# Kernel tuning notes

Measured on AMD Instinct MI355X. Metric: run time of the kernel, lower is better.

Reference implementation:

```python
import jax, jax.numpy as jnp
import numpy as np

B, S, DIM = 2, 1024, 1024
E, K, INTER = 16, 2, 512
SHARED_INTER = 2 * INTER  # n_shared_experts * moe_inter_dim
ROUTE_SCALE = 1.0


def setup_inputs() -> dict:
    key = jax.random.key(0)
    ks = jax.random.split(key, 8)
    init = lambda k, shape: jax.random.normal(k, shape, dtype=jnp.float32) * 0.02
    return {
        "x": jax.random.normal(ks[0], (B, S, DIM), dtype=jnp.float32),
        "gate_w": init(ks[1], (E, DIM)),
        "w1": init(ks[2], (E, INTER, DIM)),
        "w2": init(ks[3], (E, DIM, INTER)),
        "w3": init(ks[4], (E, INTER, DIM)),
        "sw1": init(ks[5], (SHARED_INTER, DIM)),
        "sw2": init(ks[6], (DIM, SHARED_INTER)),
        "sw3": init(ks[7], (SHARED_INTER, DIM)),
    }


def reference(x, gate_w, w1, w2, w3, sw1, sw2, sw3):
    b, s, d = x.shape
    xt = x.reshape(-1, d)            # [T, D] flattened tokens
    T = xt.shape[0]

    # Gate: sigmoid scores, top-k experts, normalize selected weights
    scores = jax.nn.sigmoid(xt @ gate_w.T)           # [T, E]
    topv, topi = jax.lax.top_k(scores, K)            # [T, K]
    weights = topv / jnp.sum(topv, axis=-1, keepdims=True) * ROUTE_SCALE

    # Per-token dense combine weights over experts: gate[t, e]
    gate = jnp.zeros((T, E), xt.dtype).at[jnp.arange(T)[:, None], topi].add(weights)

    # Routed experts (SwiGLU), computed densely and combined with gate weights
    h = jax.nn.silu(jnp.einsum('td,eid->tei', xt, w1)) * jnp.einsum('td,eid->tei', xt, w3)
    expert_out = jnp.einsum('tei,edi->ted', h, w2)   # [T, E, D]
    y = jnp.einsum('ted,te->td', expert_out, gate)   # [T, D]

    # Shared expert (SwiGLU MLP over all tokens)
    z = (jax.nn.silu(xt @ sw1.T) * (xt @ sw3.T)) @ sw2.T

    return (y + z).reshape(b, s, d)
```

## Files before the change

### kernel.cpp

```cpp
#include <hip/hip_runtime.h>
#include <stdint.h>

typedef unsigned short u16;
typedef __bf16 bf16x8 __attribute__((ext_vector_type(8)));
typedef float f32x4 __attribute__((ext_vector_type(4)));

#define TTOK 2048
#define DIMSZ 1024
#define NROUT 16
#define INTERSZ 512

__device__ __forceinline__ u16 f2bf(float f) {
    unsigned int u = __builtin_bit_cast(unsigned int, f);
    unsigned int r = u + 0x7FFFu + ((u >> 16) & 1u);
    return (u16)(r >> 16);
}

__device__ __forceinline__ void gl2lds16(const void* g, void* l) {
    __builtin_amdgcn_global_load_lds(
        (const __attribute__((address_space(1))) void*)(uintptr_t)g,
        (__attribute__((address_space(3))) void*)(uintptr_t)l,
        16, 0, 0);
}

#define NA4 (NROUT * INTERSZ * DIMSZ / 4)
#define NB4 (DIMSZ * DIMSZ / 4)
#define NR4 (NA4 + NB4)
__global__ void cast_all(const float* __restrict__ w1, const float* __restrict__ sw1,
                         const float* __restrict__ w3, const float* __restrict__ sw3,
                         const float* __restrict__ w2, const float* __restrict__ sw2,
                         u16* __restrict__ W1b, u16* __restrict__ W3b,
                         u16* __restrict__ W2b) {
    const int n4 = 3 * NR4;
    for (int i = blockIdx.x * blockDim.x + threadIdx.x; i < n4;
         i += gridDim.x * blockDim.x) {
        int r = i / NR4;
        int j = i - r * NR4;
        const float* a; const float* b; u16* d;
        if (r == 0)      { a = w1; b = sw1; d = W1b; }
        else if (r == 1) { a = w3; b = sw3; d = W3b; }
        else             { a = w2; b = sw2; d = W2b; }
        float4 v = (j < NA4) ? ((const float4*)a)[j] : ((const float4*)b)[j - NA4];
        ushort4 o;
        o.x = f2bf(v.x); o.y = f2bf(v.y); o.z = f2bf(v.z); o.w = f2bf(v.w);
        *(ushort4*)&d[(size_t)j * 4] = o;
    }
}

__global__ __launch_bounds__(256) void gate_score(
    const float* __restrict__ x, const float* __restrict__ gw,
    int* __restrict__ topi, float2* __restrict__ topw, u16* __restrict__ Xbf) {
    const int t = blockIdx.x;
    const int tid = threadIdx.x;
    const int wave = tid >> 6, lane = tid & 63;
    const int d0 = tid * 4;
    float4 xv = *(const float4*)(x + (size_t)t * DIMSZ + d0);
    ushort4 o;
    o.x = f2bf(xv.x); o.y = f2bf(xv.y); o.z = f2bf(xv.z); o.w = f2bf(xv.w);
    *(ushort4*)&Xbf[(size_t)t * DIMSZ + d0] = o;

    float acc[16];
    #pragma unroll
    for (int e = 0; e < 16; ++e) {
        float4 g = *(const float4*)(gw + e * DIMSZ + d0);
        acc[e] = xv.x * g.x + xv.y * g.y + xv.z * g.z + xv.w * g.w;
    }
    #pragma unroll
    for (int off = 32; off > 0; off >>= 1) {
        #pragma unroll
        for (int e = 0; e < 16; ++e) acc[e] += __shfl_xor(acc[e], off);
    }
    __shared__ float part[4][16];
    __shared__ float sfin[16];
    if (lane < 16) part[wave][lane] = acc[lane];
    __syncthreads();
    if (wave == 0 && lane < 16) {
        float s = part[0][lane] + part[1][lane] + part[2][lane] + part[3][lane];
        sfin[lane] = 1.f / (1.f + expf(-s));
    }
    __syncthreads();
    if (tid == 0) {
        int i0 = 0; float v0 = sfin[0];
        #pragma unroll
        for (int e = 1; e < 16; ++e) { float v = sfin[e]; if (v > v0) { v0 = v; i0 = e; } }
        int i1 = -1; float v1 = -1e30f;
        #pragma unroll
        for (int e = 0; e < 16; ++e) { float v = sfin[e]; if (e != i0 && v > v1) { v1 = v; i1 = e; } }
        float inv = 1.f / (v0 + v1);
        topi[t] = i0 | (i1 << 8);
        topw[t] = make_float2(v0 * inv, v1 * inv);
    }
}

__global__ __launch_bounds__(256) void route_kernel(
    const int* __restrict__ topi, const float2* __restrict__ topw,
    int* __restrict__ counts, int* __restrict__ tokidx, float* __restrict__ tokw) {
    const int e = blockIdx.x;
    const int tid = threadIdx.x;
    int p[8]; int m[8]; int cnt = 0;
    #pragma unroll
    for (int j = 0; j < 8; ++j) {
        int t = tid * 8 + j;
        p[j] = topi[t];
        m[j] = ((p[j] & 255) == e) || ((p[j] >> 8) == e) ? 1 : 0;
        cnt += m[j];
    }
    const int lane = tid & 63, wave = tid >> 6;
    int v = cnt;
    #pragma unroll
    for (int off = 1; off < 64; off <<= 1) {
        int u = __shfl_up(v, off);
        if (lane >= off) v += u;
    }
    __shared__ int wsum[4];
    if (lane == 63) wsum[wave] = v;
    __syncthreads();
    int wbase = 0;
    #pragma unroll
    for (int w = 0; w < 4; ++w) wbase += (w < wave) ? wsum[w] : 0;
    int base = wbase + v - cnt;
    #pragma unroll
    for (int j = 0; j < 8; ++j) {
        if (m[j]) {
            int t = tid * 8 + j;
            float2 w2 = topw[t];
            tokidx[e * TTOK + base] = t;
            tokw[e * TTOK + base] = ((p[j] & 255) == e) ? w2.x : w2.y;
            ++base;
        }
    }
    if (tid == 0) counts[e] = wsum[0] + wsum[1] + wsum[2] + wsum[3];
}

__global__ __launch_bounds__(256) void gemm1s(
    const u16* __restrict__ Xbf, const u16* __restrict__ W1b,
    const u16* __restrict__ W3b, const int* __restrict__ counts,
    const int* __restrict__ tokidx, const float* __restrict__ tokw,
    u16* __restrict__ Hc, u16* __restrict__ Hs) {
    const int e = blockIdx.z;
    const int cnt = (e < NROUT) ? counts[e] : TTOK;
    const int m0 = blockIdx.y * 64;
    if (m0 >= cnt) return;
    const int n0 = blockIdx.x * 64;
    __shared__ u16 As[64 * 64], B1s[64 * 64], B3s[64 * 64];
    const size_t eoff = (size_t)e * INTERSZ * DIMSZ;
    const u16* B1 = W1b + eoff + (size_t)n0 * DIMSZ;
    const u16* B3 = W3b + eoff + (size_t)n0 * DIMSZ;
    const int tid = threadIdx.x;

    int rowi[2], cgsi[2]; size_t arow[2];
    #pragma unroll
    for (int i = 0; i < 2; ++i) {
        int c = tid + i * 256;
        rowi[i] = c >> 3;
        cgsi[i] = ((c & 7) ^ (rowi[i] & 7)) * 8;
        int slot = m0 + rowi[i];
        int g;
        if (e < NROUT) g = (slot < cnt) ? tokidx[e * TTOK + slot] : 0;
        else           g = slot;
        arow[i] = (size_t)g * DIMSZ;
    }
    f32x4 acc1[2][2] = {}; f32x4 acc3[2][2] = {};
    const int wave = tid >> 6, lane = tid & 63;
    const int wm = (wave >> 1) * 32, wn = (wave & 1) * 32;
    const int lr = lane & 15, lq = lane >> 4;

    for (int kt = 0; kt < DIMSZ / 64; ++kt) {
        const int k0 = kt * 64;
        #pragma unroll
        for (int i = 0; i < 2; ++i) {
            int c = tid + i * 256;
            int boff = rowi[i] * DIMSZ + k0 + cgsi[i];
            gl2lds16(Xbf + arow[i] + k0 + cgsi[i], &As[c * 8]);
            gl2lds16(B1 + boff, &B1s[c * 8]);
            gl2lds16(B3 + boff, &B3s[c * 8]);
        }
        __syncthreads();
        #pragma unroll
        for (int ks = 0; ks < 2; ++ks) {
            bf16x8 af[2], b1f[2], b3f[2];
            const int g = lq + ks * 4;
            #pragma unroll
            for (int mt = 0; mt < 2; ++mt) {
                int m = wm + mt * 16 + lr;
                af[mt] = *(const bf16x8*)&As[(m * 8 + (g ^ (m & 7))) * 8];
            }
            #pragma unroll
            for (int nt = 0; nt < 2; ++nt) {
                int n = wn + nt * 16 + lr;
                int ch = (n * 8 + (g ^ (n & 7))) * 8;
                b1f[nt] = *(const bf16x8*)&B1s[ch];
                b3f[nt] = *(const bf16x8*)&B3s[ch];
            }
            #pragma unroll
            for (int mt = 0; mt < 2; ++mt) {
                #pragma unroll
                for (int nt = 0; nt < 2; ++nt) {
                    acc1[mt][nt] = __builtin_amdgcn_mfma_f32_16x16x32_bf16(af[mt], b1f[nt], acc1[mt][nt], 0, 0, 0);
                    acc3[mt][nt] = __builtin_amdgcn_mfma_f32_16x16x32_bf16(af[mt], b3f[nt], acc3[mt][nt], 0, 0, 0);
                }
            }
        }
        __syncthreads();
    }
    #pragma unroll
    for (int mt = 0; mt < 2; ++mt) {
        #pragma unroll
        for (int nt = 0; nt < 2; ++nt) {
            #pragma unroll
            for (int r = 0; r < 4; ++r) {
                int m = wm + mt * 16 + lq * 4 + r;
                int n = wn + nt * 16 + lr;
                int slot = m0 + m;
                bool valid = slot < cnt;
                float h1 = acc1[mt][nt][r], h3 = acc3[mt][nt][r];
                float hv = 0.f;
                if (valid) {
                    float tw = (e < NROUT) ? tokw[e * TTOK + slot] : 1.0f;
                    hv = h1 / (1.f + __expf(-h1)) * h3 * tw;
                }
                if (e < NROUT)
                    Hc[((size_t)e * TTOK + slot) * INTERSZ + n0 + n] = f2bf(hv);
                else
                    Hs[(size_t)slot * DIMSZ + (e - NROUT) * INTERSZ + n0 + n] = f2bf(hv);
            }
        }
    }
}

__global__ __launch_bounds__(256) void gemm2_shared(
    const u16* __restrict__ Hs, const u16* __restrict__ W2sb,
    float* __restrict__ out) {
    __shared__ u16 As[64 * 64], Bs[64 * 64];
    const int m0 = blockIdx.y * 64, n0 = blockIdx.x * 64;
    const u16* A0 = Hs + (size_t)m0 * DIMSZ;
    const u16* B0 = W2sb + (size_t)n0 * DIMSZ;
    const int tid = threadIdx.x;
    const int wave = tid >> 6, lane = tid & 63;
    const int wm = (wave >> 1) * 32, wn = (wave & 1) * 32;
    const int lr = lane & 15, lq = lane >> 4;

    f32x4 acc[2][2] = {};
    for (int kt = 0; kt < DIMSZ / 64; ++kt) {
        const int k0 = kt * 64;
        #pragma unroll
        for (int i = 0; i < 2; ++i) {
            int c = tid + i * 256;
            int row = c >> 3;
            int cgs = ((c & 7) ^ (row & 7)) * 8;
            gl2lds16(A0 + (size_t)row * DIMSZ + k0 + cgs, &As[c * 8]);
            gl2lds16(B0 + (size_t)row * DIMSZ + k0 + cgs, &Bs[c * 8]);
        }
        __syncthreads();
        #pragma unroll
        for (int ks = 0; ks < 2; ++ks) {
            bf16x8 af[2], bfr[2];
            const int g = lq + ks * 4;
            #pragma unroll
            for (int mt = 0; mt < 2; ++mt) {
                int m = wm + mt * 16 + lr;
                af[mt] = *(const bf16x8*)&As[(m * 8 + (g ^ (m & 7))) * 8];
            }
            #pragma unroll
            for (int nt = 0; nt < 2; ++nt) {
                int n = wn + nt * 16 + lr;
                bfr[nt] = *(const bf16x8*)&Bs[(n * 8 + (g ^ (n & 7))) * 8];
            }
            #pragma unroll
            for (int mt = 0; mt < 2; ++mt) {
                #pragma unroll
                for (int nt = 0; nt < 2; ++nt) {
                    acc[mt][nt] = __builtin_amdgcn_mfma_f32_16x16x32_bf16(af[mt], bfr[nt], acc[mt][nt], 0, 0, 0);
                }
            }
        }
        __syncthreads();
    }
    #pragma unroll
    for (int mt = 0; mt < 2; ++mt) {
        #pragma unroll
        for (int nt = 0; nt < 2; ++nt) {
            #pragma unroll
            for (int r = 0; r < 4; ++r) {
                int m = wm + mt * 16 + lq * 4 + r;
                int n = wn + nt * 16 + lr;
                out[(size_t)(m0 + m) * DIMSZ + n0 + n] = acc[mt][nt][r];
            }
        }
    }
}

__global__ __launch_bounds__(256) void gemm2_routed(
    const u16* __restrict__ Hc, const u16* __restrict__ W2b,
    const int* __restrict__ counts, const int* __restrict__ tokidx,
    float* __restrict__ out) {
    const int e = blockIdx.z;
    const int cnt = counts[e];
    const int m0 = blockIdx.y * 64;
    if (m0 >= cnt) return;
    const int n0 = blockIdx.x * 64;
    __shared__ u16 As[64 * 64], Bs[64 * 64];
    const u16* A0 = Hc + ((size_t)e * TTOK + m0) * INTERSZ;
    const u16* B0 = W2b + ((size_t)e * DIMSZ + n0) * INTERSZ;
    const int tid = threadIdx.x;
    const int wave = tid >> 6, lane = tid & 63;
    const int wm = (wave >> 1) * 32, wn = (wave & 1) * 32;
    const int lr = lane & 15, lq = lane >> 4;

    f32x4 acc[2][2] = {};
    for (int kt = 0; kt < INTERSZ / 64; ++kt) {
        const int k0 = kt * 64;
        #pragma unroll
        for (int i = 0; i < 2; ++i) {
            int c = tid + i * 256;
            int row = c >> 3;
            int cgs = ((c & 7) ^ (row & 7)) * 8;
            gl2lds16(A0 + (size_t)row * INTERSZ + k0 + cgs, &As[c * 8]);
            gl2lds16(B0 + (size_t)row * INTERSZ + k0 + cgs, &Bs[c * 8]);
        }
        __syncthreads();
        #pragma unroll
        for (int ks = 0; ks < 2; ++ks) {
            bf16x8 af[2], bfr[2];
            const int g = lq + ks * 4;
            #pragma unroll
            for (int mt = 0; mt < 2; ++mt) {
                int m = wm + mt * 16 + lr;
                af[mt] = *(const bf16x8*)&As[(m * 8 + (g ^ (m & 7))) * 8];
            }
            #pragma unroll
            for (int nt = 0; nt < 2; ++nt) {
                int n = wn + nt * 16 + lr;
                bfr[nt] = *(const bf16x8*)&Bs[(n * 8 + (g ^ (n & 7))) * 8];
            }
            #pragma unroll
            for (int mt = 0; mt < 2; ++mt) {
                #pragma unroll
                for (int nt = 0; nt < 2; ++nt) {
                    acc[mt][nt] = __builtin_amdgcn_mfma_f32_16x16x32_bf16(af[mt], bfr[nt], acc[mt][nt], 0, 0, 0);
                }
            }
        }
        __syncthreads();
    }
    #pragma unroll
    for (int mt = 0; mt < 2; ++mt) {
        #pragma unroll
        for (int r = 0; r < 4; ++r) {
            int m = wm + mt * 16 + lq * 4 + r;
            int slot = m0 + m;
            if (slot < cnt) {
                int t = tokidx[e * TTOK + slot];
                #pragma unroll
                for (int nt = 0; nt < 2; ++nt) {
                    int n = wn + nt * 16 + lr;
                    unsafeAtomicAdd(&out[(size_t)t * DIMSZ + n0 + n], acc[mt][nt][r]);
                }
            }
        }
    }
}

extern "C" void kernel_launch(void* const* d_in, const int* in_sizes, int n_in,
                              void* d_out, int out_size, void* d_ws, size_t ws_size,
                              hipStream_t stream) {
    const float* x      = (const float*)d_in[0];
    const float* gate_w = (const float*)d_in[1];
    const float* w1     = (const float*)d_in[2];
    const float* w2     = (const float*)d_in[3];
    const float* w3     = (const float*)d_in[4];
    const float* sw1    = (const float*)d_in[5];
    const float* sw2    = (const float*)d_in[6];
    const float* sw3    = (const float*)d_in[7];
    float* out = (float*)d_out;

    char* ws = (char*)d_ws;
    const size_t SZ_W   = (size_t)(NROUT + 2) * INTERSZ * DIMSZ * 2;
    const size_t SZ_XBF = (size_t)TTOK * DIMSZ * 2;
    u16*   W1b    = (u16*)(ws);
    u16*   W3b    = (u16*)(ws + SZ_W);
    u16*   W2all  = (u16*)(ws + 2 * SZ_W);
    u16*   Xbf    = (u16*)(ws + 3 * SZ_W);
    char*  route  = ws + 3 * SZ_W + SZ_XBF;
    int*   counts = (int*)route;
    int*   topi   = (int*)(route + 256);
    float2* topw  = (float2*)(route + 256 + TTOK * 4);
    int*   tokidx = (int*)(route + 256 + TTOK * 12);
    float* tokw   = (float*)(route + 256 + TTOK * 12 + 16 * TTOK * 4);
    char*  hbuf   = route + 256 + TTOK * 12 + 2 * (size_t)16 * TTOK * 4;
    u16*   Hc     = (u16*)hbuf;
    u16*   Hs     = (u16*)(hbuf + (size_t)NROUT * TTOK * INTERSZ * 2);
    u16*   W2sb   = W2all + (size_t)NROUT * DIMSZ * INTERSZ;

    cast_all<<<8192, 256, 0, stream>>>(w1, sw1, w3, sw3, w2, sw2, W1b, W3b, W2all);
    gate_score<<<TTOK, 256, 0, stream>>>(x, gate_w, topi, topw, Xbf);
    route_kernel<<<NROUT, 256, 0, stream>>>(topi, topw, counts, tokidx, tokw);
    gemm1s<<<dim3(INTERSZ / 64, TTOK / 64, NROUT + 2), 256, 0, stream>>>(
        Xbf, W1b, W3b, counts, tokidx, tokw, Hc, Hs);
    gemm2_shared<<<dim3(DIMSZ / 64, TTOK / 64), 256, 0, stream>>>(Hs, W2sb, out);
    gemm2_routed<<<dim3(DIMSZ / 64, TTOK / 64, NROUT), 256, 0, stream>>>(
        Hc, W2all, counts, tokidx, out);
}
```

Measured before the change: 238.5 us.

## Widen gemm1 N-tile, merge shared and routed gemm2 kernels, vectorize weight cast

gemm1s now computes a 64x128 tile per block, reusing each gathered activation tile across twice as many output columns and halving the number of redundant A loads. The shared and routed second GEMMs are merged into one launch that accumulates with atomics into an output zeroed by a memset, so they can run concurrently instead of back-to-back. The weight cast kernel uses a 2D grid with one row per weight group and 8-element vector stores, which removes the per-element division. The changes add register and LDS pressure in gemm1, atomic traffic for the shared expert, and one extra memset.

```diff
diff --git a/kernel.cpp b/kernel.cpp
--- a/kernel.cpp
+++ b/kernel.cpp
@@ -4,6 +4,7 @@
 typedef unsigned short u16;
 typedef __bf16 bf16x8 __attribute__((ext_vector_type(8)));
 typedef float f32x4 __attribute__((ext_vector_type(4)));
+typedef unsigned short u16x8 __attribute__((ext_vector_type(8)));
 
 #define TTOK 2048
 #define DIMSZ 1024
@@ -25,25 +26,27 @@
 
 #define NA4 (NROUT * INTERSZ * DIMSZ / 4)
 #define NB4 (DIMSZ * DIMSZ / 4)
-#define NR4 (NA4 + NB4)
+#define NA8 (NA4 / 2)
+#define NR8 ((NA4 + NB4) / 2)
 __global__ void cast_all(const float* __restrict__ w1, const float* __restrict__ sw1,
                          const float* __restrict__ w3, const float* __restrict__ sw3,
                          const float* __restrict__ w2, const float* __restrict__ sw2,
                          u16* __restrict__ W1b, u16* __restrict__ W3b,
                          u16* __restrict__ W2b) {
-    const int n4 = 3 * NR4;
-    for (int i = blockIdx.x * blockDim.x + threadIdx.x; i < n4;
-         i += gridDim.x * blockDim.x) {
-        int r = i / NR4;
-        int j = i - r * NR4;
-        const float* a; const float* b; u16* d;
-        if (r == 0)      { a = w1; b = sw1; d = W1b; }
-        else if (r == 1) { a = w3; b = sw3; d = W3b; }
-        else             { a = w2; b = sw2; d = W2b; }
-        float4 v = (j < NA4) ? ((const float4*)a)[j] : ((const float4*)b)[j - NA4];
-        ushort4 o;
-        o.x = f2bf(v.x); o.y = f2bf(v.y); o.z = f2bf(v.z); o.w = f2bf(v.w);
-        *(ushort4*)&d[(size_t)j * 4] = o;
+    const int r = blockIdx.y;
+    const float* a; const float* b; u16* d;
+    if (r == 0)      { a = w1; b = sw1; d = W1b; }
+    else if (r == 1) { a = w3; b = sw3; d = W3b; }
+    else             { a = w2; b = sw2; d = W2b; }
+    for (int j = blockIdx.x * blockDim.x + threadIdx.x; j < NR8;
+         j += gridDim.x * blockDim.x) {
+        const float4* src = (j < NA8) ? (const float4*)a + 2 * (size_t)j
+                                      : (const float4*)b + 2 * (size_t)(j - NA8);
+        float4 v0 = src[0], v1 = src[1];
+        u16x8 o;
+        o[0] = f2bf(v0.x); o[1] = f2bf(v0.y); o[2] = f2bf(v0.z); o[3] = f2bf(v0.w);
+        o[4] = f2bf(v1.x); o[5] = f2bf(v1.y); o[6] = f2bf(v1.z); o[7] = f2bf(v1.w);
+        *(u16x8*)&d[(size_t)j * 8] = o;
     }
 }
 
@@ -141,28 +144,35 @@
     const int cnt = (e < NROUT) ? counts[e] : TTOK;
     const int m0 = blockIdx.y * 64;
     if (m0 >= cnt) return;
-    const int n0 = blockIdx.x * 64;
-    __shared__ u16 As[64 * 64], B1s[64 * 64], B3s[64 * 64];
+    const int n0 = blockIdx.x * 128;
+    __shared__ u16 As[64 * 64], B1s[128 * 64], B3s[128 * 64];
     const size_t eoff = (size_t)e * INTERSZ * DIMSZ;
     const u16* B1 = W1b + eoff + (size_t)n0 * DIMSZ;
     const u16* B3 = W3b + eoff + (size_t)n0 * DIMSZ;
     const int tid = threadIdx.x;
 
-    int rowi[2], cgsi[2]; size_t arow[2];
+    int rowa[2], cgsa[2]; size_t arow[2];
     #pragma unroll
     for (int i = 0; i < 2; ++i) {
         int c = tid + i * 256;
-        rowi[i] = c >> 3;
-        cgsi[i] = ((c & 7) ^ (rowi[i] & 7)) * 8;
-        int slot = m0 + rowi[i];
+        rowa[i] = c >> 3;
+        cgsa[i] = ((c & 7) ^ (rowa[i] & 7)) * 8;
+        int slot = m0 + rowa[i];
         int g;
         if (e < NROUT) g = (slot < cnt) ? tokidx[e * TTOK + slot] : 0;
         else           g = slot;
         arow[i] = (size_t)g * DIMSZ;
     }
-    f32x4 acc1[2][2] = {}; f32x4 acc3[2][2] = {};
+    int rowb[4], cgsb[4];
+    #pragma unroll
+    for (int i = 0; i < 4; ++i) {
+        int c = tid + i * 256;
+        rowb[i] = c >> 3;
+        cgsb[i] = ((c & 7) ^ (rowb[i] & 7)) * 8;
+    }
+    f32x4 acc1[2][4] = {}; f32x4 acc3[2][4] = {};
     const int wave = tid >> 6, lane = tid & 63;
-    const int wm = (wave >> 1) * 32, wn = (wave & 1) * 32;
+    const int wm = (wave >> 1) * 32, wn = (wave & 1) * 64;
     const int lr = lane & 15, lq = lane >> 4;
 
     for (int kt = 0; kt < DIMSZ / 64; ++kt) {
@@ -170,15 +180,19 @@
         #pragma unroll
         for (int i = 0; i < 2; ++i) {
             int c = tid + i * 256;
-            int boff = rowi[i] * DIMSZ + k0 + cgsi[i];
-            gl2lds16(Xbf + arow[i] + k0 + cgsi[i], &As[c * 8]);
+            gl2lds16(Xbf + arow[i] + k0 + cgsa[i], &As[c * 8]);
+        }
+        #pragma unroll
+        for (int i = 0; i < 4; ++i) {
+            int c = tid + i * 256;
+            int boff = rowb[i] * DIMSZ + k0 + cgsb[i];
             gl2lds16(B1 + boff, &B1s[c * 8]);
             gl2lds16(B3 + boff, &B3s[c * 8]);
         }
         __syncthreads();
         #pragma unroll
         for (int ks = 0; ks < 2; ++ks) {
-            bf16x8 af[2], b1f[2], b3f[2];
+            bf16x8 af[2], b1f[4], b3f[4];
             const int g = lq + ks * 4;
             #pragma unroll
             for (int mt = 0; mt < 2; ++mt) {
@@ -186,7 +200,7 @@
                 af[mt] = *(const bf16x8*)&As[(m * 8 + (g ^ (m & 7))) * 8];
             }
             #pragma unroll
-            for (int nt = 0; nt < 2; ++nt) {
+            for (int nt = 0; nt < 4; ++nt) {
                 int n = wn + nt * 16 + lr;
                 int ch = (n * 8 + (g ^ (n & 7))) * 8;
                 b1f[nt] = *(const bf16x8*)&B1s[ch];
@@ -195,7 +209,7 @@
             #pragma unroll
             for (int mt = 0; mt < 2; ++mt) {
                 #pragma unroll
-                for (int nt = 0; nt < 2; ++nt) {
+                for (int nt = 0; nt < 4; ++nt) {
                     acc1[mt][nt] = __builtin_amdgcn_mfma_f32_16x16x32_bf16(af[mt], b1f[nt], acc1[mt][nt], 0, 0, 0);
                     acc3[mt][nt] = __builtin_amdgcn_mfma_f32_16x16x32_bf16(af[mt], b3f[nt], acc3[mt][nt], 0, 0, 0);
                 }
@@ -206,7 +220,7 @@
     #pragma unroll
     for (int mt = 0; mt < 2; ++mt) {
         #pragma unroll
-        for (int nt = 0; nt < 2; ++nt) {
+        for (int nt = 0; nt < 4; ++nt) {
             #pragma unroll
             for (int r = 0; r < 4; ++r) {
                 int m = wm + mt * 16 + lq * 4 + r;
@@ -228,28 +242,44 @@
     }
 }
 
-__global__ __launch_bounds__(256) void gemm2_shared(
-    const u16* __restrict__ Hs, const u16* __restrict__ W2sb,
+__global__ __launch_bounds__(256) void gemm2u(
+    const u16* __restrict__ Hc, const u16* __restrict__ Hs,
+    const u16* __restrict__ W2b, const u16* __restrict__ W2sb,
+    const int* __restrict__ counts, const int* __restrict__ tokidx,
     float* __restrict__ out) {
+    const int e = blockIdx.z;
+    const bool routed = (e < NROUT);
+    const int cnt = routed ? counts[e] : TTOK;
+    const int m0 = blockIdx.y * 64;
+    if (m0 >= cnt) return;
+    const int n0 = blockIdx.x * 64;
+    const int klen = routed ? INTERSZ : DIMSZ;
     __shared__ u16 As[64 * 64], Bs[64 * 64];
-    const int m0 = blockIdx.y * 64, n0 = blockIdx.x * 64;
-    const u16* A0 = Hs + (size_t)m0 * DIMSZ;
-    const u16* B0 = W2sb + (size_t)n0 * DIMSZ;
+    const u16* A0 = routed ? Hc + ((size_t)e * TTOK + m0) * INTERSZ
+                           : Hs + (size_t)m0 * DIMSZ;
+    const u16* B0 = routed ? W2b + ((size_t)e * DIMSZ + n0) * INTERSZ
+                           : W2sb + (size_t)n0 * DIMSZ;
     const int tid = threadIdx.x;
     const int wave = tid >> 6, lane = tid & 63;
     const int wm = (wave >> 1) * 32, wn = (wave & 1) * 32;
     const int lr = lane & 15, lq = lane >> 4;
 
+    int rowi[2], cgsi[2];
+    #pragma unroll
+    for (int i = 0; i < 2; ++i) {
+        int c = tid + i * 256;
+        rowi[i] = c >> 3;
+        cgsi[i] = ((c & 7) ^ (rowi[i] & 7)) * 8;
+    }
+
     f32x4 acc[2][2] = {};
-    for (int kt = 0; kt < DIMSZ / 64; ++kt) {
+    for (int kt = 0; kt < klen / 64; ++kt) {
         const int k0 = kt * 64;
         #pragma unroll
         for (int i = 0; i < 2; ++i) {
             int c = tid + i * 256;
-            int row = c >> 3;
-            int cgs = ((c & 7) ^ (row & 7)) * 8;
-            gl2lds16(A0 + (size_t)row * DIMSZ + k0 + cgs, &As[c * 8]);
-            gl2lds16(B0 + (size_t)row * DIMSZ + k0 + cgs, &Bs[c * 8]);
+            gl2lds16(A0 + (size_t)rowi[i] * klen + k0 + cgsi[i], &As[c * 8]);
+            gl2lds16(B0 + (size_t)rowi[i] * klen + k0 + cgsi[i], &Bs[c * 8]);
         }
         __syncthreads();
         #pragma unroll
@@ -279,78 +309,11 @@
     #pragma unroll
     for (int mt = 0; mt < 2; ++mt) {
         #pragma unroll
-        for (int nt = 0; nt < 2; ++nt) {
-            #pragma unroll
-            for (int r = 0; r < 4; ++r) {
-                int m = wm + mt * 16 + lq * 4 + r;
-                int n = wn + nt * 16 + lr;
-                out[(size_t)(m0 + m) * DIMSZ + n0 + n] = acc[mt][nt][r];
-            }
-        }
-    }
-}
-
-__global__ __launch_bounds__(256) void gemm2_routed(
-    const u16* __restrict__ Hc, const u16* __restrict__ W2b,
-    const int* __restrict__ counts, const int* __restrict__ tokidx,
-    float* __restrict__ out) {
-    const int e = blockIdx.z;
-    const int cnt = counts[e];
-    const int m0 = blockIdx.y * 64;
-    if (m0 >= cnt) return;
-    const int n0 = blockIdx.x * 64;
-    __shared__ u16 As[64 * 64], Bs[64 * 64];
-    const u16* A0 = Hc + ((size_t)e * TTOK + m0) * INTERSZ;
-    const u16* B0 = W2b + ((size_t)e * DIMSZ + n0) * INTERSZ;
-    const int tid = threadIdx.x;
-    const int wave = tid >> 6, lane = tid & 63;
-    const int wm = (wave >> 1) * 32, wn = (wave & 1) * 32;
-    const int lr = lane & 15, lq = lane >> 4;
-
-    f32x4 acc[2][2] = {};
-    for (int kt = 0; kt < INTERSZ / 64; ++kt) {
-        const int k0 = kt * 64;
-        #pragma unroll
-        for (int i = 0; i < 2; ++i) {
-            int c = tid + i * 256;
-            int row = c >> 3;
-            int cgs = ((c & 7) ^ (row & 7)) * 8;
-            gl2lds16(A0 + (size_t)row * INTERSZ + k0 + cgs, &As[c * 8]);
-            gl2lds16(B0 + (size_t)row * INTERSZ + k0 + cgs, &Bs[c * 8]);
-        }
-        __syncthreads();
-        #pragma unroll
-        for (int ks = 0; ks < 2; ++ks) {
-            bf16x8 af[2], bfr[2];
-            const int g = lq + ks * 4;
-            #pragma unroll
-            for (int mt = 0; mt < 2; ++mt) {
-                int m = wm + mt * 16 + lr;
-                af[mt] = *(const bf16x8*)&As[(m * 8 + (g ^ (m & 7))) * 8];
-            }
-            #pragma unroll
-            for (int nt = 0; nt < 2; ++nt) {
-                int n = wn + nt * 16 + lr;
-                bfr[nt] = *(const bf16x8*)&Bs[(n * 8 + (g ^ (n & 7))) * 8];
-            }
-            #pragma unroll
-            for (int mt = 0; mt < 2; ++mt) {
-                #pragma unroll
-                for (int nt = 0; nt < 2; ++nt) {
-                    acc[mt][nt] = __builtin_amdgcn_mfma_f32_16x16x32_bf16(af[mt], bfr[nt], acc[mt][nt], 0, 0, 0);
-                }
-            }
-        }
-        __syncthreads();
-    }
-    #pragma unroll
-    for (int mt = 0; mt < 2; ++mt) {
-        #pragma unroll
         for (int r = 0; r < 4; ++r) {
             int m = wm + mt * 16 + lq * 4 + r;
             int slot = m0 + m;
             if (slot < cnt) {
-                int t = tokidx[e * TTOK + slot];
+                int t = routed ? tokidx[e * TTOK + slot] : slot;
                 #pragma unroll
                 for (int nt = 0; nt < 2; ++nt) {
                     int n = wn + nt * 16 + lr;
@@ -392,12 +355,12 @@
     u16*   Hs     = (u16*)(hbuf + (size_t)NROUT * TTOK * INTERSZ * 2);
     u16*   W2sb   = W2all + (size_t)NROUT * DIMSZ * INTERSZ;
 
-    cast_all<<<8192, 256, 0, stream>>>(w1, sw1, w3, sw3, w2, sw2, W1b, W3b, W2all);
+    hipMemsetAsync(out, 0, (size_t)TTOK * DIMSZ * 4, stream);
+    cast_all<<<dim3(2048, 3), 256, 0, stream>>>(w1, sw1, w3, sw3, w2, sw2, W1b, W3b, W2all);
     gate_score<<<TTOK, 256, 0, stream>>>(x, gate_w, topi, topw, Xbf);
     route_kernel<<<NROUT, 256, 0, stream>>>(topi, topw, counts, tokidx, tokw);
-    gemm1s<<<dim3(INTERSZ / 64, TTOK / 64, NROUT + 2), 256, 0, stream>>>(
+    gemm1s<<<dim3(INTERSZ / 128, TTOK / 64, NROUT + 2), 256, 0, stream>>>(
         Xbf, W1b, W3b, counts, tokidx, tokw, Hc, Hs);
-    gemm2_shared<<<dim3(DIMSZ / 64, TTOK / 64), 256, 0, stream>>>(Hs, W2sb, out);
-    gemm2_routed<<<dim3(DIMSZ / 64, TTOK / 64, NROUT), 256, 0, stream>>>(
-        Hc, W2all, counts, tokidx, out);
-}
+    gemm2u<<<dim3(DIMSZ / 64, TTOK / 64, NROUT + 1), 256, 0, stream>>>(
+        Hc, Hs, W2all, W2sb, counts, tokidx, out);
+}
```

New measurement: 237.0 us. Within noise of the previous version (-0.6%).
